# Optimization experiments

Hardware: AMD Instinct MI355X
Metric: run time of the kernel (lower is better)

The kernel has to match this reference:

```python
import jax, jax.numpy as jnp
from jax import lax
import numpy as np

KSIZE = 5  # kernel_size from init
CHANNEL = 256

def _gaussian_kernel2d(sigma, ksize):
    # matches torch: exp(-i^2/(2*sigma^2)) outer product, normalized to sum 1
    n = ksize // 2
    r = jnp.arange(-n, n + 1, dtype=jnp.float32)
    g = jnp.exp(-(r ** 2) / (2.0 * sigma ** 2))
    k2d = g[:, None] * g[None, :]
    return k2d / k2d.sum()

def setup_inputs() -> dict:
    key = jax.random.key(0)
    k1, k2 = jax.random.split(key)
    x = jax.random.normal(k1, (16, CHANNEL, 64, 64), dtype=jnp.float32)
    # sigma is the module's learned scalar; keep away from 0 for a well-defined kernel
    sigma = jax.random.uniform(k2, (1,), dtype=jnp.float32, minval=0.5, maxval=1.5)
    return {"x": x, "sigma": sigma}

def reference(x, sigma):
    # The torch module writes a channel-diagonal weight into a dense Conv2d;
    # mathematically this is a depthwise conv with the same 2D Gaussian per channel.
    C = x.shape[1]
    k2d = _gaussian_kernel2d(sigma[0], KSIZE)
    w = jnp.broadcast_to(k2d[None, None, :, :], (C, 1, KSIZE, KSIZE))  # OIHW, groups=C
    pad = KSIZE // 2
    return lax.conv_general_dilated(
        x, w,
        window_strides=(1, 1),
        padding=[(pad, pad), (pad, pad)],
        dimension_numbers=("NCHW", "OIHW", "NCHW"),
        feature_group_count=C,
    )
```

## Files before the change

kernel.cpp:

```cpp
#include <hip/hip_runtime.h>
#include <math.h>


constexpr int Hh   = 64;
constexpr int Ww   = 64;
constexpr int KS   = 5;
constexpr int PADc = 2;
constexpr int TH   = Hh + 2 * PADc;
constexpr int IN_STR  = 72;
constexpr int TMP_STR = 64;

__global__ __launch_bounds__(256, 4) void gauss5(const float* __restrict__ x,
                                                 const float* __restrict__ sigma,
                                                 float* __restrict__ out) {
    __shared__ float sIn[TH * IN_STR];
    __shared__ float sTmp[TH * TMP_STR];

    const int t = threadIdx.x;
    const size_t plane = blockIdx.x;
    const float* __restrict__ xp = x + plane * (size_t)(Hh * Ww);
    float* __restrict__ op = out + plane * (size_t)(Hh * Ww);

    const float sg = sigma[0];
    const float c2 = -1.0f / (2.0f * sg * sg);
    float g[KS];
    float gsum = 0.0f;
#pragma unroll
    for (int i = 0; i < KS; ++i) {
        float d = (float)(i - PADc);
        g[i] = expf(d * d * c2);
        gsum += g[i];
    }
    const float ginv = 1.0f / gsum;
#pragma unroll
    for (int i = 0; i < KS; ++i) g[i] *= ginv;

    for (int i = t; i < TH * IN_STR; i += 256) sIn[i] = 0.0f;
    __syncthreads();

    const float4* __restrict__ x4 = (const float4*)xp;
#pragma unroll
    for (int k = 0; k < 4; ++k) {
        int idx = t + k * 256;
        int r   = idx >> 4;
        int c   = (idx & 15) << 2;
        float4 v = x4[idx];
        float* dst = &sIn[(r + PADc) * IN_STR + c + PADc];
        dst[0] = v.x; dst[1] = v.y; dst[2] = v.z; dst[3] = v.w;
    }
    __syncthreads();

    for (int idx = t; idx < TH * (Ww / 4); idx += 256) {
        int r  = idx >> 4;
        int c4 = idx & 15;
        const float* src = &sIn[r * IN_STR + (c4 << 2)];
        float4 a = *(const float4*)(src);
        float4 b = *(const float4*)(src + 4);
        float f0 = a.x, f1 = a.y, f2 = a.z, f3 = a.w;
        float f4 = b.x, f5 = b.y, f6 = b.z, f7 = b.w;
        float4 o;
        o.x = g[0]*f0 + g[1]*f1 + g[2]*f2 + g[3]*f3 + g[4]*f4;
        o.y = g[0]*f1 + g[1]*f2 + g[2]*f3 + g[3]*f4 + g[4]*f5;
        o.z = g[0]*f2 + g[1]*f3 + g[2]*f4 + g[3]*f5 + g[4]*f6;
        o.w = g[0]*f3 + g[1]*f4 + g[2]*f5 + g[3]*f6 + g[4]*f7;
        *(float4*)&sTmp[r * TMP_STR + (c4 << 2)] = o;
    }
    __syncthreads();

    float4* __restrict__ o4 = (float4*)op;
#pragma unroll
    for (int k = 0; k < 4; ++k) {
        int idx = t + k * 256;
        int r   = idx >> 4;
        int c4  = idx & 15;
        const float* base = &sTmp[r * TMP_STR + (c4 << 2)];
        float4 acc = make_float4(0.f, 0.f, 0.f, 0.f);
#pragma unroll
        for (int j = 0; j < KS; ++j) {
            float4 v = *(const float4*)(base + j * TMP_STR);
            acc.x += g[j] * v.x;
            acc.y += g[j] * v.y;
            acc.z += g[j] * v.z;
            acc.w += g[j] * v.w;
        }
        o4[idx] = acc;
    }
}

extern "C" void kernel_launch(void* const* d_in, const int* in_sizes, int n_in,
                              void* d_out, int out_size, void* d_ws, size_t ws_size,
                              hipStream_t stream) {
    const float* x     = (const float*)d_in[0];
    const float* sigma = (const float*)d_in[1];
    float* out         = (float*)d_out;
    const int planes = in_sizes[0] / (Hh * Ww);
    gauss5<<<planes, 256, 0, stream>>>(x, sigma, out);
}
```

Before: 113.7 us.

## Keep horizontal pass in registers and zero only the halo of shared tile

Each thread now computes the horizontal blur for 8 consecutive rows in registers and reuses them for 4 vertical outputs. This removes the sTmp shared buffer and one barrier. Only the padding border of the input tile is zeroed, and that zeroing overlaps the interior load, which drops a second barrier. Halving shared memory and raising launch bounds to 6 allows more blocks per CU. In exchange the horizontal pass is partly recomputed (8 rows per 4 outputs) and each thread holds more registers.

```diff
diff --git a/kernel.cpp b/kernel.cpp
--- a/kernel.cpp
+++ b/kernel.cpp
@@ -7,14 +7,12 @@
 constexpr int KS   = 5;
 constexpr int PADc = 2;
 constexpr int TH   = Hh + 2 * PADc;
-constexpr int IN_STR  = 72;
-constexpr int TMP_STR = 64;
+constexpr int IN_STR = 72;
 
-__global__ __launch_bounds__(256, 4) void gauss5(const float* __restrict__ x,
+__global__ __launch_bounds__(256, 6) void gauss5(const float* __restrict__ x,
                                                  const float* __restrict__ sigma,
                                                  float* __restrict__ out) {
     __shared__ float sIn[TH * IN_STR];
-    __shared__ float sTmp[TH * TMP_STR];
 
     const int t = threadIdx.x;
     const size_t plane = blockIdx.x;
@@ -35,8 +33,20 @@
 #pragma unroll
     for (int i = 0; i < KS; ++i) g[i] *= ginv;
 
-    for (int i = t; i < TH * IN_STR; i += 256) sIn[i] = 0.0f;
-    __syncthreads();
+    for (int i = t; i < 528; i += 256) {
+        if (i < 272) {
+            int rr  = i / 68;
+            int cc  = i - rr * 68;
+            int row = (rr < 2) ? rr : (rr + 64);
+            sIn[row * IN_STR + cc] = 0.0f;
+        } else {
+            int j   = i - 272;
+            int row = 2 + (j >> 2);
+            int k   = j & 3;
+            int col = (k < 2) ? k : (k + 64);
+            sIn[row * IN_STR + col] = 0.0f;
+        }
+    }
 
     const float4* __restrict__ x4 = (const float4*)xp;
 #pragma unroll
@@ -50,40 +60,35 @@
     }
     __syncthreads();
 
-    for (int idx = t; idx < TH * (Ww / 4); idx += 256) {
-        int r  = idx >> 4;
-        int c4 = idx & 15;
-        const float* src = &sIn[r * IN_STR + (c4 << 2)];
+    const int c4 = t & 15;
+    const int r0 = (t >> 4) << 2;
+
+    float4 h[8];
+#pragma unroll
+    for (int i = 0; i < 8; ++i) {
+        const float* src = &sIn[(r0 + i) * IN_STR + (c4 << 2)];
         float4 a = *(const float4*)(src);
         float4 b = *(const float4*)(src + 4);
-        float f0 = a.x, f1 = a.y, f2 = a.z, f3 = a.w;
-        float f4 = b.x, f5 = b.y, f6 = b.z, f7 = b.w;
-        float4 o;
-        o.x = g[0]*f0 + g[1]*f1 + g[2]*f2 + g[3]*f3 + g[4]*f4;
-        o.y = g[0]*f1 + g[1]*f2 + g[2]*f3 + g[3]*f4 + g[4]*f5;
-        o.z = g[0]*f2 + g[1]*f3 + g[2]*f4 + g[3]*f5 + g[4]*f6;
-        o.w = g[0]*f3 + g[1]*f4 + g[2]*f5 + g[3]*f6 + g[4]*f7;
-        *(float4*)&sTmp[r * TMP_STR + (c4 << 2)] = o;
+        h[i].x = g[0]*a.x + g[1]*a.y + g[2]*a.z + g[3]*a.w + g[4]*b.x;
+        h[i].y = g[0]*a.y + g[1]*a.z + g[2]*a.w + g[3]*b.x + g[4]*b.y;
+        h[i].z = g[0]*a.z + g[1]*a.w + g[2]*b.x + g[3]*b.y + g[4]*b.z;
+        h[i].w = g[0]*a.w + g[1]*b.x + g[2]*b.y + g[3]*b.z + g[4]*b.w;
     }
-    __syncthreads();
 
     float4* __restrict__ o4 = (float4*)op;
 #pragma unroll
-    for (int k = 0; k < 4; ++k) {
-        int idx = t + k * 256;
-        int r   = idx >> 4;
-        int c4  = idx & 15;
-        const float* base = &sTmp[r * TMP_STR + (c4 << 2)];
-        float4 acc = make_float4(0.f, 0.f, 0.f, 0.f);
+    for (int i = 0; i < 4; ++i) {
+        float4 acc;
+        acc.x = g[0]*h[i].x; acc.y = g[0]*h[i].y;
+        acc.z = g[0]*h[i].z; acc.w = g[0]*h[i].w;
 #pragma unroll
-        for (int j = 0; j < KS; ++j) {
-            float4 v = *(const float4*)(base + j * TMP_STR);
-            acc.x += g[j] * v.x;
-            acc.y += g[j] * v.y;
-            acc.z += g[j] * v.z;
-            acc.w += g[j] * v.w;
+        for (int j = 1; j < KS; ++j) {
+            acc.x += g[j] * h[i+j].x;
+            acc.y += g[j] * h[i+j].y;
+            acc.z += g[j] * h[i+j].z;
+            acc.w += g[j] * h[i+j].w;
         }
-        o4[idx] = acc;
+        o4[(r0 + i) * 16 + c4] = acc;
     }
 }
 
```

Result: slower. 118.7 us (+4.3%).

## Replace shared-memory separable blur with register-resident wave-per-plane shuffle version

Applied to the files above, without the earlier changes.

Each 64-lane wavefront now handles a whole 64x64 plane, and each lane owns a 4-wide column strip of 16 rows. Horizontal neighbours come from cross-lane shuffles and the vertical pass runs entirely in registers, so LDS staging, zero-fill and block barriers are gone. In exchange, halo rows are re-read from global memory (20 loads per 16 output rows), register pressure is higher and launch bounds drop to 2. The grid shrinks to planes/4, which assumes the plane count is divisible by 4.

```diff
diff --git a/kernel.cpp b/kernel.cpp
--- a/kernel.cpp
+++ b/kernel.cpp
@@ -2,88 +2,79 @@
 #include <math.h>
 
 
-constexpr int Hh   = 64;
-constexpr int Ww   = 64;
-constexpr int KS   = 5;
+constexpr int Hh = 64;
+constexpr int Ww = 64;
+constexpr int KS = 5;
 constexpr int PADc = 2;
-constexpr int TH   = Hh + 2 * PADc;
-constexpr int IN_STR  = 72;
-constexpr int TMP_STR = 64;
 
-__global__ __launch_bounds__(256, 4) void gauss5(const float* __restrict__ x,
+__global__ __launch_bounds__(256, 2) void gauss5(const float* __restrict__ x,
                                                  const float* __restrict__ sigma,
                                                  float* __restrict__ out) {
-    __shared__ float sIn[TH * IN_STR];
-    __shared__ float sTmp[TH * TMP_STR];
+    const int t    = threadIdx.x;
+    const int lane = t & 63;
+    const int wid  = t >> 6;
+    const size_t plane = (size_t)blockIdx.x * 4 + wid;
 
-    const int t = threadIdx.x;
-    const size_t plane = blockIdx.x;
-    const float* __restrict__ xp = x + plane * (size_t)(Hh * Ww);
-    float* __restrict__ op = out + plane * (size_t)(Hh * Ww);
+    const int c4  = lane & 15;
+    const int g16 = (lane >> 4) << 4;
 
     const float sg = sigma[0];
     const float c2 = -1.0f / (2.0f * sg * sg);
-    float g[KS];
-    float gsum = 0.0f;
+    float w[KS];
+    float wsum = 0.0f;
 #pragma unroll
     for (int i = 0; i < KS; ++i) {
         float d = (float)(i - PADc);
-        g[i] = expf(d * d * c2);
-        gsum += g[i];
+        w[i] = expf(d * d * c2);
+        wsum += w[i];
     }
-    const float ginv = 1.0f / gsum;
+    const float winv = 1.0f / wsum;
 #pragma unroll
-    for (int i = 0; i < KS; ++i) g[i] *= ginv;
+    for (int i = 0; i < KS; ++i) w[i] *= winv;
 
-    for (int i = t; i < TH * IN_STR; i += 256) sIn[i] = 0.0f;
-    __syncthreads();
+    const float4* __restrict__ x4 = (const float4*)(x + plane * (Hh * Ww));
+    float4* __restrict__ o4       = (float4*)(out + plane * (Hh * Ww));
 
-    const float4* __restrict__ x4 = (const float4*)xp;
+    const int lm1 = lane - 1;
+    const int lp1 = lane + 1;
+    const bool leftEdge  = (c4 == 0);
+    const bool rightEdge = (c4 == 15);
+
+    float4 h[20];
 #pragma unroll
-    for (int k = 0; k < 4; ++k) {
-        int idx = t + k * 256;
-        int r   = idx >> 4;
-        int c   = (idx & 15) << 2;
-        float4 v = x4[idx];
-        float* dst = &sIn[(r + PADc) * IN_STR + c + PADc];
-        dst[0] = v.x; dst[1] = v.y; dst[2] = v.z; dst[3] = v.w;
+    for (int i = 0; i < 20; ++i) {
+        int ri = g16 - PADc + i;
+        int rc = ri < 0 ? 0 : (ri > 63 ? 63 : ri);
+        float4 v = x4[rc * 16 + c4];
+        if (ri != rc) { v.x = 0.f; v.y = 0.f; v.z = 0.f; v.w = 0.f; }
+
+        float lz = __shfl(v.z, lm1, 64);
+        float lw = __shfl(v.w, lm1, 64);
+        float rx = __shfl(v.x, lp1, 64);
+        float ry = __shfl(v.y, lp1, 64);
+        lz = leftEdge  ? 0.f : lz;
+        lw = leftEdge  ? 0.f : lw;
+        rx = rightEdge ? 0.f : rx;
+        ry = rightEdge ? 0.f : ry;
+
+        h[i].x = w[0]*lz  + w[1]*lw  + w[2]*v.x + w[3]*v.y + w[4]*v.z;
+        h[i].y = w[0]*lw  + w[1]*v.x + w[2]*v.y + w[3]*v.z + w[4]*v.w;
+        h[i].z = w[0]*v.x + w[1]*v.y + w[2]*v.z + w[3]*v.w + w[4]*rx;
+        h[i].w = w[0]*v.y + w[1]*v.z + w[2]*v.w + w[3]*rx  + w[4]*ry;
     }
-    __syncthreads();
 
-    for (int idx = t; idx < TH * (Ww / 4); idx += 256) {
-        int r  = idx >> 4;
-        int c4 = idx & 15;
-        const float* src = &sIn[r * IN_STR + (c4 << 2)];
-        float4 a = *(const float4*)(src);
-        float4 b = *(const float4*)(src + 4);
-        float f0 = a.x, f1 = a.y, f2 = a.z, f3 = a.w;
-        float f4 = b.x, f5 = b.y, f6 = b.z, f7 = b.w;
-        float4 o;
-        o.x = g[0]*f0 + g[1]*f1 + g[2]*f2 + g[3]*f3 + g[4]*f4;
-        o.y = g[0]*f1 + g[1]*f2 + g[2]*f3 + g[3]*f4 + g[4]*f5;
-        o.z = g[0]*f2 + g[1]*f3 + g[2]*f4 + g[3]*f5 + g[4]*f6;
-        o.w = g[0]*f3 + g[1]*f4 + g[2]*f5 + g[3]*f6 + g[4]*f7;
-        *(float4*)&sTmp[r * TMP_STR + (c4 << 2)] = o;
-    }
-    __syncthreads();
-
-    float4* __restrict__ o4 = (float4*)op;
 #pragma unroll
-    for (int k = 0; k < 4; ++k) {
-        int idx = t + k * 256;
-        int r   = idx >> 4;
-        int c4  = idx & 15;
-        const float* base = &sTmp[r * TMP_STR + (c4 << 2)];
-        float4 acc = make_float4(0.f, 0.f, 0.f, 0.f);
+    for (int r = 0; r < 16; ++r) {
+        float4 a;
+        a.x = w[0]*h[r].x; a.y = w[0]*h[r].y; a.z = w[0]*h[r].z; a.w = w[0]*h[r].w;
 #pragma unroll
-        for (int j = 0; j < KS; ++j) {
-            float4 v = *(const float4*)(base + j * TMP_STR);
-            acc.x += g[j] * v.x;
-            acc.y += g[j] * v.y;
-            acc.z += g[j] * v.z;
-            acc.w += g[j] * v.w;
+        for (int j = 1; j < KS; ++j) {
+            a.x += w[j] * h[r + j].x;
+            a.y += w[j] * h[r + j].y;
+            a.z += w[j] * h[r + j].z;
+            a.w += w[j] * h[r + j].w;
         }
-        o4[idx] = acc;
+        o4[(g16 + r) * 16 + c4] = a;
     }
 }
 
@@ -94,5 +85,5 @@
     const float* sigma = (const float*)d_in[1];
     float* out         = (float*)d_out;
     const int planes = in_sizes[0] / (Hh * Ww);
-    gauss5<<<planes, 256, 0, stream>>>(x, sigma, out);
+    gauss5<<<planes / 4, 256, 0, stream>>>(x, sigma, out);
 }
```

Result: slower. 117.6 us (+3.5%).
